# Kernel tuning notes

Measured on AMD Instinct MI355X. Metric: run time of the kernel, lower is better.

Reference implementation:

```python
import jax, jax.numpy as jnp
import numpy as np
from jax import lax

H = 20  # hidden_size


def _rnn_layer(x_seq, h0, W_ih, W_hh, b_ih, b_hh):
    """Vanilla tanh RNN layer. x_seq: [B,T,D], h0: [B,H]. Returns ([B,T,H], [B,H])."""
    # Precompute input projection for all timesteps (the only large GEMM).
    xp = jnp.einsum('btd,hd->bth', x_seq, W_ih) + b_ih + b_hh  # [B,T,H]

    def step(h, xt):
        h = jnp.tanh(xt + h @ W_hh.T)
        return h, h

    h_last, hs = lax.scan(step, h0, jnp.swapaxes(xp, 0, 1))  # hs: [T,B,H]
    return jnp.swapaxes(hs, 0, 1), h_last


def setup_inputs() -> dict:
    key = jax.random.key(0)
    ks = jax.random.split(key, 12)
    B, T = 4096, 512
    s = 1.0 / np.sqrt(H)  # PyTorch default uniform(-1/sqrt(H), 1/sqrt(H))
    u = lambda k, shape: jax.random.uniform(k, shape, jnp.float32, -s, s)
    return {
        'x': jax.random.normal(ks[0], (B, T, 1), jnp.float32),
        'hidden': jax.random.normal(ks[1], (2, B, H), jnp.float32),
        'W_ih0': u(ks[2], (H, 1)),
        'W_hh0': u(ks[3], (H, H)),
        'b_ih0': u(ks[4], (H,)),
        'b_hh0': u(ks[5], (H,)),
        'W_ih1': u(ks[6], (H, H)),
        'W_hh1': u(ks[7], (H, H)),
        'b_ih1': u(ks[8], (H,)),
        'b_hh1': u(ks[9], (H,)),
        'fc_w': u(ks[10], (1, H)),
        'fc_b': u(ks[11], (1,)),
    }


def reference(x, hidden, W_ih0, W_hh0, b_ih0, b_hh0, W_ih1, W_hh1, b_ih1, b_hh1, fc_w, fc_b):
    # 2-layer vanilla RNN (eval mode: inter-layer dropout disabled)
    h0_seq, h0_last = _rnn_layer(x, hidden[0], W_ih0, W_hh0, b_ih0, b_hh0)
    h1_seq, h1_last = _rnn_layer(h0_seq, hidden[1], W_ih1, W_hh1, b_ih1, b_hh1)
    out = h1_seq[:, -1, :] @ fc_w.T + fc_b  # [B,1]
    new_hidden = jnp.stack([h0_last, h1_last], axis=0)  # [2,B,H]
    return out, new_hidden
```

## Files before the change

### kernel.cpp

```cpp
#include <hip/hip_runtime.h>


#define Bsz 4096
#define Tn  512
#define Hn  20
#define GB  3
#define XPAD 520
#define NTHREADS 64

typedef float v2 __attribute__((ext_vector_type(2)));

__device__ __forceinline__ float tanh_fast(float v) {
    float e = __expf(2.0f * v);
    return 1.0f - 2.0f * __builtin_amdgcn_rcpf(e + 1.0f);
}

#define DOT20P(acc, accb, W, H) do { \
    acc  = __builtin_elementwise_fma(W##0, H##0, acc);  \
    accb = __builtin_elementwise_fma(W##1, H##1, accb); \
    acc  = __builtin_elementwise_fma(W##2, H##2, acc);  \
    accb = __builtin_elementwise_fma(W##3, H##3, accb); \
    acc  = __builtin_elementwise_fma(W##4, H##4, acc);  \
    accb = __builtin_elementwise_fma(W##5, H##5, accb); \
    acc  = __builtin_elementwise_fma(W##6, H##6, acc);  \
    accb = __builtin_elementwise_fma(W##7, H##7, accb); \
    acc  = __builtin_elementwise_fma(W##8, H##8, acc);  \
    accb = __builtin_elementwise_fma(W##9, H##9, accb); \
} while (0)

#define LOAD_ROWP(W, ptr) \
    v2 W##0, W##1, W##2, W##3, W##4, W##5, W##6, W##7, W##8, W##9; \
    { const float4* _p = (const float4*)(ptr); \
      float4 _t; \
      _t = _p[0]; W##0 = (v2){_t.x, _t.y}; W##1 = (v2){_t.z, _t.w}; \
      _t = _p[1]; W##2 = (v2){_t.x, _t.y}; W##3 = (v2){_t.z, _t.w}; \
      _t = _p[2]; W##4 = (v2){_t.x, _t.y}; W##5 = (v2){_t.z, _t.w}; \
      _t = _p[3]; W##6 = (v2){_t.x, _t.y}; W##7 = (v2){_t.z, _t.w}; \
      _t = _p[4]; W##8 = (v2){_t.x, _t.y}; W##9 = (v2){_t.z, _t.w}; }

#define READ_H(H, base) \
    v2 H##0, H##1, H##2, H##3, H##4, H##5, H##6, H##7, H##8, H##9; \
    { const float4 _a = *(const float4*)((base) + 0);  \
      const float4 _b = *(const float4*)((base) + 4);  \
      const float4 _c = *(const float4*)((base) + 8);  \
      const float4 _d = *(const float4*)((base) + 12); \
      const float4 _e = *(const float4*)((base) + 16); \
      H##0 = (v2){_a.x, _a.y}; H##1 = (v2){_a.z, _a.w}; \
      H##2 = (v2){_b.x, _b.y}; H##3 = (v2){_b.z, _b.w}; \
      H##4 = (v2){_c.x, _c.y}; H##5 = (v2){_c.z, _c.w}; \
      H##6 = (v2){_d.x, _d.y}; H##7 = (v2){_d.z, _d.w}; \
      H##8 = (v2){_e.x, _e.y}; H##9 = (v2){_e.z, _e.w}; }

__global__ __launch_bounds__(NTHREADS)
__attribute__((amdgpu_waves_per_eu(1, 2)))
void rnn2_fused(const float* __restrict__ x,
                const float* __restrict__ hidden,
                const float* __restrict__ W_ih0,
                const float* __restrict__ W_hh0,
                const float* __restrict__ b_ih0,
                const float* __restrict__ b_hh0,
                const float* __restrict__ W_ih1,
                const float* __restrict__ W_hh1,
                const float* __restrict__ b_ih1,
                const float* __restrict__ b_hh1,
                const float* __restrict__ fc_w,
                const float* __restrict__ fc_b,
                float* __restrict__ out)
{
    const int tid = threadIdx.x;
    int g = tid / Hn;
    int j = tid - g * Hn;
    const bool lane_ok = (tid < GB * Hn);
    if (!lane_ok) g = GB - 1;
    const int  b        = blockIdx.x * GB + g;
    const bool b_ok     = (b < Bsz);
    const int  bl       = b_ok ? b : (Bsz - 1);
    const bool store_ok = lane_ok && b_ok;

    __shared__ float xs[GB][XPAD];
    __shared__ float hs[2][GB][Hn];

    LOAD_ROWP(w0, W_hh0 + j * Hn)
    LOAD_ROWP(w1, W_ih1 + j * Hn)
    LOAD_ROWP(w2, W_hh1 + j * Hn)

    const float wih0  = W_ih0[j];
    const float bias0 = b_ih0[j] + b_hh0[j];
    const float bias1 = b_ih1[j] + b_hh1[j];

    {
        const int bB = blockIdx.x * GB;
        #pragma unroll
        for (int r = 0; r < (GB * Tn) / (NTHREADS * 4); ++r) {
            const int c  = (r * NTHREADS + tid) * 4;
            const int gg = c >> 9;
            const int t  = c & (Tn - 1);
            const int bb = (bB + gg < Bsz) ? (bB + gg) : (Bsz - 1);
            float4 v = *(const float4*)(x + (long)bb * Tn + t);
            *(float4*)&xs[gg][t] = v;
        }
    }

    hs[0][g][j] = hidden[bl * Hn + j];
    hs[1][g][j] = hidden[(long)Bsz * Hn + bl * Hn + j];

    {
        READ_H(hA, &hs[0][g][0])
        v2 a0  = (v2){fmaf(xs[g][0], wih0, bias0), 0.f};
        v2 a0b = (v2){0.f, 0.f};
        DOT20P(a0, a0b, w0, hA);
        v2 s0 = a0 + a0b;
        hs[0][g][j] = tanh_fast(s0.x + s0.y);
    }

    #pragma unroll 4
    for (int i = 1; i < Tn; ++i) {
        READ_H(hA, &hs[0][g][0])
        READ_H(hB, &hs[1][g][0])

        const float xt = xs[g][i];

        v2 a0  = (v2){fmaf(xt, wih0, bias0), 0.f};
        v2 a0b = (v2){0.f, 0.f};
        v2 a1  = (v2){bias1, 0.f};
        v2 a1b = (v2){0.f, 0.f};
        v2 a2  = (v2){0.f, 0.f};
        v2 a2b = (v2){0.f, 0.f};
        DOT20P(a0, a0b, w0, hA);
        DOT20P(a1, a1b, w1, hA);
        DOT20P(a2, a2b, w2, hB);

        const v2 s0 = a0 + a0b;
        const v2 s1 = (a1 + a1b) + (a2 + a2b);
        const float n0 = tanh_fast(s0.x + s0.y);
        const float n1 = tanh_fast(s1.x + s1.y);
        hs[0][g][j] = n0;
        hs[1][g][j] = n1;
    }

    {
        READ_H(hA, &hs[0][g][0])
        READ_H(hB, &hs[1][g][0])
        v2 a1  = (v2){bias1, 0.f};
        v2 a1b = (v2){0.f, 0.f};
        v2 a2  = (v2){0.f, 0.f};
        v2 a2b = (v2){0.f, 0.f};
        DOT20P(a1, a1b, w1, hA);
        DOT20P(a2, a2b, w2, hB);
        const v2 s1 = (a1 + a1b) + (a2 + a2b);
        hs[1][g][j] = tanh_fast(s1.x + s1.y);
    }

    if (store_ok) {
        out[Bsz + (long)b * Hn + j]                  = hs[0][g][j];
        out[Bsz + (long)Bsz * Hn + (long)b * Hn + j] = hs[1][g][j];
        if (j == 0) {
            LOAD_ROWP(fw, fc_w)
            READ_H(hv, &hs[1][g][0])
            v2 aA = (v2){fc_b[0], 0.f};
            v2 aB = (v2){0.f, 0.f};
            DOT20P(aA, aB, fw, hv);
            const v2 s = aA + aB;
            out[b] = s.x + s.y;
        }
    }
}

extern "C" void kernel_launch(void* const* d_in, const int* in_sizes, int n_in,
                              void* d_out, int out_size, void* d_ws, size_t ws_size,
                              hipStream_t stream) {
    const float* x      = (const float*)d_in[0];
    const float* hidden = (const float*)d_in[1];
    const float* W_ih0  = (const float*)d_in[2];
    const float* W_hh0  = (const float*)d_in[3];
    const float* b_ih0  = (const float*)d_in[4];
    const float* b_hh0  = (const float*)d_in[5];
    const float* W_ih1  = (const float*)d_in[6];
    const float* W_hh1  = (const float*)d_in[7];
    const float* b_ih1  = (const float*)d_in[8];
    const float* b_hh1  = (const float*)d_in[9];
    const float* fc_w   = (const float*)d_in[10];
    const float* fc_b   = (const float*)d_in[11];

    const int nblocks = (Bsz + GB - 1) / GB;
    rnn2_fused<<<nblocks, NTHREADS, 0, stream>>>(
        x, hidden, W_ih0, W_hh0, b_ih0, b_hh0,
        W_ih1, W_hh1, b_ih1, b_hh1, fc_w, fc_b, (float*)d_out);
}
```

Measured before the change: 129.4 us.

## Overlap layer-0 LDS hidden-state read with layer-1 dot products in recurrence

Restructures the time loop so the layer-0 step runs first and writes its new hidden state to shared memory. The layer-1 step then runs on register-held copies of the previous hidden states while the fresh layer-0 state is read back into a temporary. Hidden vectors now persist in registers across iterations instead of being re-read at the top of each step, so LDS latency is hidden behind independent FMA work. The unroll factor drops from 4 to 2, likely to offset the extra register pressure from the temporary hidden copies. The final hidden output now comes from a register value.

Result: slower. 140.4 us (+8.4%).

```diff
diff --git a/kernel.cpp b/kernel.cpp
--- a/kernel.cpp
+++ b/kernel.cpp
@@ -38,18 +38,25 @@
       _t = _p[3]; W##6 = (v2){_t.x, _t.y}; W##7 = (v2){_t.z, _t.w}; \
       _t = _p[4]; W##8 = (v2){_t.x, _t.y}; W##9 = (v2){_t.z, _t.w}; }
 
-#define READ_H(H, base) \
-    v2 H##0, H##1, H##2, H##3, H##4, H##5, H##6, H##7, H##8, H##9; \
-    { const float4 _a = *(const float4*)((base) + 0);  \
-      const float4 _b = *(const float4*)((base) + 4);  \
-      const float4 _c = *(const float4*)((base) + 8);  \
-      const float4 _d = *(const float4*)((base) + 12); \
-      const float4 _e = *(const float4*)((base) + 16); \
-      H##0 = (v2){_a.x, _a.y}; H##1 = (v2){_a.z, _a.w}; \
-      H##2 = (v2){_b.x, _b.y}; H##3 = (v2){_b.z, _b.w}; \
-      H##4 = (v2){_c.x, _c.y}; H##5 = (v2){_c.z, _c.w}; \
-      H##6 = (v2){_d.x, _d.y}; H##7 = (v2){_d.z, _d.w}; \
-      H##8 = (v2){_e.x, _e.y}; H##9 = (v2){_e.z, _e.w}; }
+#define DECL_H(H) v2 H##0, H##1, H##2, H##3, H##4, H##5, H##6, H##7, H##8, H##9;
+
+#define READ_INTO(H, base) do { \
+    const float4 _a = *(const float4*)((base) + 0);  \
+    const float4 _b = *(const float4*)((base) + 4);  \
+    const float4 _c = *(const float4*)((base) + 8);  \
+    const float4 _d = *(const float4*)((base) + 12); \
+    const float4 _e = *(const float4*)((base) + 16); \
+    H##0 = (v2){_a.x, _a.y}; H##1 = (v2){_a.z, _a.w}; \
+    H##2 = (v2){_b.x, _b.y}; H##3 = (v2){_b.z, _b.w}; \
+    H##4 = (v2){_c.x, _c.y}; H##5 = (v2){_c.z, _c.w}; \
+    H##6 = (v2){_d.x, _d.y}; H##7 = (v2){_d.z, _d.w}; \
+    H##8 = (v2){_e.x, _e.y}; H##9 = (v2){_e.z, _e.w}; \
+} while (0)
+
+#define COPY_H(D, S) do { \
+    D##0=S##0; D##1=S##1; D##2=S##2; D##3=S##3; D##4=S##4; \
+    D##5=S##5; D##6=S##6; D##7=S##7; D##8=S##8; D##9=S##9; \
+} while (0)
 
 __global__ __launch_bounds__(NTHREADS)
 __attribute__((amdgpu_waves_per_eu(1, 2)))
@@ -104,43 +111,31 @@
     hs[0][g][j] = hidden[bl * Hn + j];
     hs[1][g][j] = hidden[(long)Bsz * Hn + bl * Hn + j];
 
+    DECL_H(hA)  DECL_H(hB)  DECL_H(hT)
+    READ_INTO(hA, &hs[0][g][0]);
+    READ_INTO(hB, &hs[1][g][0]);
+
     {
-        READ_H(hA, &hs[0][g][0])
         v2 a0  = (v2){fmaf(xs[g][0], wih0, bias0), 0.f};
         v2 a0b = (v2){0.f, 0.f};
         DOT20P(a0, a0b, w0, hA);
-        v2 s0 = a0 + a0b;
+        const v2 s0 = a0 + a0b;
         hs[0][g][j] = tanh_fast(s0.x + s0.y);
-    }
-
-    #pragma unroll 4
+        READ_INTO(hT, &hs[0][g][0]);
+        COPY_H(hA, hT);
+    }
+
+    #pragma unroll 2
     for (int i = 1; i < Tn; ++i) {
-        READ_H(hA, &hs[0][g][0])
-        READ_H(hB, &hs[1][g][0])
-
         const float xt = xs[g][i];
 
         v2 a0  = (v2){fmaf(xt, wih0, bias0), 0.f};
         v2 a0b = (v2){0.f, 0.f};
-        v2 a1  = (v2){bias1, 0.f};
-        v2 a1b = (v2){0.f, 0.f};
-        v2 a2  = (v2){0.f, 0.f};
-        v2 a2b = (v2){0.f, 0.f};
         DOT20P(a0, a0b, w0, hA);
-        DOT20P(a1, a1b, w1, hA);
-        DOT20P(a2, a2b, w2, hB);
-
         const v2 s0 = a0 + a0b;
-        const v2 s1 = (a1 + a1b) + (a2 + a2b);
-        const float n0 = tanh_fast(s0.x + s0.y);
-        const float n1 = tanh_fast(s1.x + s1.y);
-        hs[0][g][j] = n0;
-        hs[1][g][j] = n1;
-    }
-
-    {
-        READ_H(hA, &hs[0][g][0])
-        READ_H(hB, &hs[1][g][0])
+        hs[0][g][j] = tanh_fast(s0.x + s0.y);
+        READ_INTO(hT, &hs[0][g][0]);
+
         v2 a1  = (v2){bias1, 0.f};
         v2 a1b = (v2){0.f, 0.f};
         v2 a2  = (v2){0.f, 0.f};
@@ -149,14 +144,30 @@
         DOT20P(a2, a2b, w2, hB);
         const v2 s1 = (a1 + a1b) + (a2 + a2b);
         hs[1][g][j] = tanh_fast(s1.x + s1.y);
+        COPY_H(hA, hT);
+        READ_INTO(hB, &hs[1][g][0]);
+    }
+
+    float n1_last;
+    {
+        v2 a1  = (v2){bias1, 0.f};
+        v2 a1b = (v2){0.f, 0.f};
+        v2 a2  = (v2){0.f, 0.f};
+        v2 a2b = (v2){0.f, 0.f};
+        DOT20P(a1, a1b, w1, hA);
+        DOT20P(a2, a2b, w2, hB);
+        const v2 s1 = (a1 + a1b) + (a2 + a2b);
+        n1_last = tanh_fast(s1.x + s1.y);
+        hs[1][g][j] = n1_last;
     }
 
     if (store_ok) {
         out[Bsz + (long)b * Hn + j]                  = hs[0][g][j];
-        out[Bsz + (long)Bsz * Hn + (long)b * Hn + j] = hs[1][g][j];
+        out[Bsz + (long)Bsz * Hn + (long)b * Hn + j] = n1_last;
         if (j == 0) {
             LOAD_ROWP(fw, fc_w)
-            READ_H(hv, &hs[1][g][0])
+            DECL_H(hv)
+            READ_INTO(hv, &hs[1][g][0]);
             v2 aA = (v2){fc_b[0], 0.f};
             v2 aB = (v2){0.f, 0.f};
             DOT20P(aA, aB, fw, hv);
```

## Split the two RNN layers across two waves with a pipelined step lag

Applied to the files above, without the earlier changes.

The block grows from one wave to two. Wave 0 computes layer 0 and wave 1 computes layer 1 one timestep behind, with the layer-0 hidden state double-buffered in LDS. This shortens the per-step dependent FMA chain each wave executes and overlaps the two layers' recurrences. In exchange it adds a block-wide barrier every timestep and doubles the number of waves launched.

Measured after the change: 133.5 us. 3.2% more time.

```diff
diff --git a/kernel.cpp b/kernel.cpp
--- a/kernel.cpp
+++ b/kernel.cpp
@@ -6,7 +6,7 @@
 #define Hn  20
 #define GB  3
 #define XPAD 520
-#define NTHREADS 64
+#define NTHREADS 128
 
 typedef float v2 __attribute__((ext_vector_type(2)));
 
@@ -52,7 +52,7 @@
       H##8 = (v2){_e.x, _e.y}; H##9 = (v2){_e.z, _e.w}; }
 
 __global__ __launch_bounds__(NTHREADS)
-__attribute__((amdgpu_waves_per_eu(1, 2)))
+__attribute__((amdgpu_waves_per_eu(1, 4)))
 void rnn2_fused(const float* __restrict__ x,
                 const float* __restrict__ hidden,
                 const float* __restrict__ W_ih0,
@@ -67,22 +67,26 @@
                 const float* __restrict__ fc_b,
                 float* __restrict__ out)
 {
-    const int tid = threadIdx.x;
-    int g = tid / Hn;
-    int j = tid - g * Hn;
-    const bool lane_ok = (tid < GB * Hn);
-    if (!lane_ok) g = GB - 1;
+    const int tid  = threadIdx.x;
+    const int wave = tid >> 6;
+    const int lane = tid & 63;
+    int g = lane / Hn;
+    int j = lane - g * Hn;
+    const bool lane_ok = (lane < GB * Hn);
+    if (!lane_ok) { g = GB - 1; j = lane - 60; }
+
     const int  b        = blockIdx.x * GB + g;
     const bool b_ok     = (b < Bsz);
     const int  bl       = b_ok ? b : (Bsz - 1);
     const bool store_ok = lane_ok && b_ok;
 
     __shared__ float xs[GB][XPAD];
-    __shared__ float hs[2][GB][Hn];
+    __shared__ float h0s[2][GB][Hn];
+    __shared__ float h1s[GB][Hn];
 
-    LOAD_ROWP(w0, W_hh0 + j * Hn)
-    LOAD_ROWP(w1, W_ih1 + j * Hn)
-    LOAD_ROWP(w2, W_hh1 + j * Hn)
+    const float* rowA = (wave == 0) ? (W_hh0 + j * Hn) : (W_ih1 + j * Hn);
+    LOAD_ROWP(wA, rowA)
+    LOAD_ROWP(wB, W_hh1 + j * Hn)
 
     const float wih0  = W_ih0[j];
     const float bias0 = b_ih0[j] + b_hh0[j];
@@ -101,67 +105,69 @@
         }
     }
 
-    hs[0][g][j] = hidden[bl * Hn + j];
-    hs[1][g][j] = hidden[(long)Bsz * Hn + bl * Hn + j];
+    if (wave == 0) h0s[1][g][j] = hidden[bl * Hn + j];
+    else           h1s[g][j]    = hidden[(long)Bsz * Hn + bl * Hn + j];
+    __syncthreads();
 
-    {
-        READ_H(hA, &hs[0][g][0])
-        v2 a0  = (v2){fmaf(xs[g][0], wih0, bias0), 0.f};
-        v2 a0b = (v2){0.f, 0.f};
-        DOT20P(a0, a0b, w0, hA);
-        v2 s0 = a0 + a0b;
-        hs[0][g][j] = tanh_fast(s0.x + s0.y);
+    float n_keep = 0.f;
+
+    #pragma unroll 2
+    for (int i = 0; i < Tn; ++i) {
+        const int p = (i + 1) & 1, q = i & 1;
+        if (wave == 0) {
+            READ_H(hA, &h0s[p][g][0])
+            const float xt = xs[g][i];
+            v2 a  = (v2){fmaf(xt, wih0, bias0), 0.f};
+            v2 ab = (v2){0.f, 0.f};
+            DOT20P(a, ab, wA, hA);
+            const v2 s = a + ab;
+            const float n = tanh_fast(s.x + s.y);
+            h0s[q][g][j] = n;
+            n_keep = n;
+        } else if (i > 0) {
+            READ_H(hA, &h0s[p][g][0])
+            READ_H(hB, &h1s[g][0])
+            v2 a1  = (v2){bias1, 0.f};
+            v2 a1b = (v2){0.f, 0.f};
+            v2 a2  = (v2){0.f, 0.f};
+            v2 a2b = (v2){0.f, 0.f};
+            DOT20P(a1, a1b, wA, hA);
+            DOT20P(a2, a2b, wB, hB);
+            const v2 s = (a1 + a1b) + (a2 + a2b);
+            const float n = tanh_fast(s.x + s.y);
+            h1s[g][j] = n;
+            n_keep = n;
+        }
+        __syncthreads();
     }
 
-    #pragma unroll 4
-    for (int i = 1; i < Tn; ++i) {
-        READ_H(hA, &hs[0][g][0])
-        READ_H(hB, &hs[1][g][0])
-
-        const float xt = xs[g][i];
-
-        v2 a0  = (v2){fmaf(xt, wih0, bias0), 0.f};
-        v2 a0b = (v2){0.f, 0.f};
+    if (wave == 0) {
+        if (store_ok)
+            out[Bsz + (long)b * Hn + j] = n_keep;
+    } else {
+        READ_H(hA, &h0s[1][g][0])
+        READ_H(hB, &h1s[g][0])
         v2 a1  = (v2){bias1, 0.f};
         v2 a1b = (v2){0.f, 0.f};
         v2 a2  = (v2){0.f, 0.f};
         v2 a2b = (v2){0.f, 0.f};
-        DOT20P(a0, a0b, w0, hA);
-        DOT20P(a1, a1b, w1, hA);
-        DOT20P(a2, a2b, w2, hB);
+        DOT20P(a1, a1b, wA, hA);
+        DOT20P(a2, a2b, wB, hB);
+        const v2 s = (a1 + a1b) + (a2 + a2b);
+        const float n1_last = tanh_fast(s.x + s.y);
+        h1s[g][j] = n1_last;
 
-        const v2 s0 = a0 + a0b;
-        const v2 s1 = (a1 + a1b) + (a2 + a2b);
-        const float n0 = tanh_fast(s0.x + s0.y);
-        const float n1 = tanh_fast(s1.x + s1.y);
-        hs[0][g][j] = n0;
-        hs[1][g][j] = n1;
-    }
-
-    {
-        READ_H(hA, &hs[0][g][0])
-        READ_H(hB, &hs[1][g][0])
-        v2 a1  = (v2){bias1, 0.f};
-        v2 a1b = (v2){0.f, 0.f};
-        v2 a2  = (v2){0.f, 0.f};
-        v2 a2b = (v2){0.f, 0.f};
-        DOT20P(a1, a1b, w1, hA);
-        DOT20P(a2, a2b, w2, hB);
-        const v2 s1 = (a1 + a1b) + (a2 + a2b);
-        hs[1][g][j] = tanh_fast(s1.x + s1.y);
-    }
-
-    if (store_ok) {
-        out[Bsz + (long)b * Hn + j]                  = hs[0][g][j];
-        out[Bsz + (long)Bsz * Hn + (long)b * Hn + j] = hs[1][g][j];
-        if (j == 0) {
-            LOAD_ROWP(fw, fc_w)
-            READ_H(hv, &hs[1][g][0])
-            v2 aA = (v2){fc_b[0], 0.f};
-            v2 aB = (v2){0.f, 0.f};
-            DOT20P(aA, aB, fw, hv);
-            const v2 s = aA + aB;
-            out[b] = s.x + s.y;
+        if (store_ok) {
+            out[Bsz + (long)Bsz * Hn + (long)b * Hn + j] = n1_last;
+            if (j == 0) {
+                LOAD_ROWP(fw, fc_w)
+                READ_H(hv, &h1s[g][0])
+                v2 aA = (v2){fc_b[0], 0.f};
+                v2 aB = (v2){0.f, 0.f};
+                DOT20P(aA, aB, fw, hv);
+                const v2 sf = aA + aB;
+                out[b] = sf.x + sf.y;
+            }
         }
     }
 }
```
